# Kernel tuning notes

Measured on AMD Instinct MI355X. Metric: run time of the kernel, lower is better.

The kernel has to match this reference:

```python
import jax, jax.numpy as jnp
import numpy as np

DIM = 384
WS = 8        # window_size
SHIFT = 4     # shift_size
HEADS = 8
HEAD_DIM = DIM // HEADS
SCALE = HEAD_DIM ** (-0.5)
EPS = 1e-5


def layernorm(x, g, b):
    m = jnp.mean(x, axis=-1, keepdims=True)
    v = jnp.var(x, axis=-1, keepdims=True)
    return (x - m) * jax.lax.rsqrt(v + EPS) * g + b


def setup_inputs() -> dict:
    key = jax.random.key(0)
    ks = jax.random.split(key, 8)
    s = 0.02
    return {
        "x": jax.random.normal(ks[0], (8, DIM, 64, 64), dtype=jnp.float32),
        "qkv_w": jax.random.normal(ks[1], (DIM, 3 * DIM), dtype=jnp.float32) * s,
        "qkv_b": jnp.zeros((3 * DIM,), jnp.float32),
        "proj_w": jax.random.normal(ks[2], (DIM, DIM), dtype=jnp.float32) * s,
        "proj_b": jnp.zeros((DIM,), jnp.float32),
        "ln1_g": jnp.ones((DIM,), jnp.float32),
        "ln1_b": jnp.zeros((DIM,), jnp.float32),
        "ln2_g": jnp.ones((DIM,), jnp.float32),
        "ln2_b": jnp.zeros((DIM,), jnp.float32),
        "mlp_w1": jax.random.normal(ks[3], (DIM, 4 * DIM), dtype=jnp.float32) * s,
        "mlp_b1": jnp.zeros((4 * DIM,), jnp.float32),
        "mlp_w2": jax.random.normal(ks[4], (4 * DIM, DIM), dtype=jnp.float32) * s,
        "mlp_b2": jnp.zeros((DIM,), jnp.float32),
    }


def reference(x, qkv_w, qkv_b, proj_w, proj_b, ln1_g, ln1_b, ln2_g, ln2_b,
              mlp_w1, mlp_b1, mlp_w2, mlp_b2):
    B, C, H, W = x.shape
    x_skip = jnp.transpose(x, (0, 2, 3, 1))  # [B,H,W,C]
    xh = x_skip
    pad_b = (-H) % WS
    pad_r = (-W) % WS
    xh = jnp.pad(xh, ((0, 0), (0, pad_b), (0, pad_r), (0, 0)))
    Hp, Wp = xh.shape[1], xh.shape[2]
    if SHIFT > 0:
        xh = jnp.roll(xh, (-SHIFT, -SHIFT), axis=(1, 2))
    # window partition -> [B*nH*nW, WS*WS, C]
    win = xh.reshape(B, Hp // WS, WS, Wp // WS, WS, C)
    win = win.transpose(0, 1, 3, 2, 4, 5).reshape(-1, WS * WS, C)
    win = layernorm(win, ln1_g, ln1_b)
    # windowed MHA (no shift mask in original module)
    Bw, N, _ = win.shape
    qkv = (win @ qkv_w + qkv_b).reshape(Bw, N, 3, HEADS, HEAD_DIM)
    qkv = qkv.transpose(2, 0, 3, 1, 4)  # [3, Bw, H, N, d]
    q, k, v = qkv[0] * SCALE, qkv[1], qkv[2]
    attn = jax.nn.softmax(jnp.einsum('bhnd,bhmd->bhnm', q, k), axis=-1)
    out = jnp.einsum('bhnm,bhmd->bhnd', attn, v)
    out = out.transpose(0, 2, 1, 3).reshape(Bw, N, C)
    out = out @ proj_w + proj_b
    # window reverse
    xh = out.reshape(B, Hp // WS, Wp // WS, WS, WS, C)
    xh = xh.transpose(0, 1, 3, 2, 4, 5).reshape(B, Hp, Wp, C)
    if SHIFT > 0:
        xh = jnp.roll(xh, (SHIFT, SHIFT), axis=(1, 2))
    xh = xh[:, :H, :W, :] + x_skip
    h = layernorm(xh, ln2_g, ln2_b)
    h = jax.nn.gelu(h @ mlp_w1 + mlp_b1, approximate=False) @ mlp_w2 + mlp_b2
    return jnp.transpose(h, (0, 3, 1, 2))  # [B,C,H,W]
```

## Files before the change

### kernel.cpp

```cpp
#include <hip/hip_runtime.h>
#include <hip/hip_bf16.h>
#include <math.h>

#define DIM   384
#define HEADS 8
#define HD    48
#define NTOK  32768
#define NWIN  512

typedef __attribute__((ext_vector_type(8))) short bf16x8;
typedef __attribute__((ext_vector_type(8))) unsigned short u16x8;
typedef __attribute__((ext_vector_type(4))) float f32x4;

__device__ __forceinline__ float bf2f(unsigned short u) {
    unsigned int v = ((unsigned int)u) << 16;
    return __uint_as_float(v);
}
__device__ __forceinline__ unsigned short f2bf(float f) {
    __bf16 b = (__bf16)f;
    return __builtin_bit_cast(unsigned short, b);
}

__device__ __forceinline__ float gelu(float v) {
    float z  = v * 0.70710678118654752f;
    float az = fabsf(z);
    float t  = __builtin_amdgcn_rcpf(1.0f + 0.47047f * az);
    float p  = t * (0.3480242f + t * (-0.0958798f + t * 0.7478556f));
    float ea = 1.0f - p * __expf(-az * az);
    float er = copysignf(ea, z);
    return 0.5f * v * (1.0f + er);
}

__device__ __forceinline__ void tok2src(int tok, int& b, int& hs, int& ws) {
    int bb  = tok >> 12;
    int win = (tok >> 6) & 63;
    int t   = tok & 63;
    int hi = win >> 3, wi = win & 7;
    int r  = t >> 3,  cc = t & 7;
    b  = bb;
    hs = (hi * 8 + r  + 4) & 63;
    ws = (wi * 8 + cc + 4) & 63;
}

__global__ __launch_bounds__(256) void k_wt4(const float* __restrict__ qkv_w,
                                             const float* __restrict__ proj_w,
                                             const float* __restrict__ w1,
                                             const float* __restrict__ w2,
                                             unsigned short* __restrict__ d0,
                                             unsigned short* __restrict__ d1,
                                             unsigned short* __restrict__ d2,
                                             unsigned short* __restrict__ d3) {
    __shared__ unsigned short T[64][66];
    int b = blockIdx.x;
    const float* W; unsigned short* Wt; int K, N, lt;
    if (b < 108)      { W = qkv_w;  Wt = d0; K = 384;  N = 1152; lt = b; }
    else if (b < 144) { W = proj_w; Wt = d1; K = 384;  N = 384;  lt = b - 108; }
    else if (b < 288) { W = w1;     Wt = d2; K = 384;  N = 1536; lt = b - 144; }
    else              { W = w2;     Wt = d3; K = 1536; N = 384;  lt = b - 288; }
    int tn = N >> 6;
    int k0 = (lt / tn) << 6, n0 = (lt % tn) << 6;
    int t  = threadIdx.x;
    int cl = t & 63, rw = t >> 6;
    #pragma unroll
    for (int p = 0; p < 16; p++) {
        int kk = p * 4 + rw;
        T[cl][kk] = f2bf(W[(size_t)(k0 + kk) * N + n0 + cl]);
    }
    __syncthreads();
    #pragma unroll
    for (int p = 0; p < 16; p++) {
        int nn = p * 4 + rw;
        Wt[(size_t)(n0 + nn) * K + k0 + cl] = T[nn][cl];
    }
}

__global__ __launch_bounds__(256) void k_ln1(const float* __restrict__ x,
                                             const float* __restrict__ g,
                                             const float* __restrict__ bt,
                                             unsigned short* __restrict__ ln1) {
    int blk = blockIdx.x;
    int b  = blk >> 6, hs = blk & 63;
    int t  = threadIdx.x;
    int w  = t & 63, cg = t >> 6;
    const float* row = x + (size_t)b * DIM * 4096 + hs * 64;

    float v[96];
    float sum = 0.f, sq = 0.f;
    #pragma unroll
    for (int i = 0; i < 96; i++) {
        int c = i * 4 + cg;
        float xv = row[(size_t)c * 4096 + w];
        v[i] = xv;
        sum += xv; sq += xv * xv;
    }
    __shared__ float red[2][4][64];
    __shared__ float mean_s[64], rstd_s[64];
    red[0][cg][w] = sum; red[1][cg][w] = sq;
    __syncthreads();
    if (t < 64) {
        float s  = red[0][0][t] + red[0][1][t] + red[0][2][t] + red[0][3][t];
        float q2 = red[1][0][t] + red[1][1][t] + red[1][2][t] + red[1][3][t];
        float mean = s * (1.0f / DIM);
        float var  = q2 * (1.0f / DIM) - mean * mean;
        mean_s[t] = mean;
        rstd_s[t] = rsqrtf(var + 1e-5f);
    }
    __syncthreads();

    int wp = t >> 2, seg = t & 3;
    int hr = (hs + 60) & 63, wr = (wp + 60) & 63;
    int tok = ((b * 8 + (hr >> 3)) * 8 + (wr >> 3)) * 64 + (hr & 7) * 8 + (wr & 7);

    __shared__ __align__(16) unsigned short tile[64][72];
    #pragma unroll
    for (int chunk = 0; chunk < 6; chunk++) {
        float mean = mean_s[w], rstd = rstd_s[w];
        #pragma unroll
        for (int it = 0; it < 16; it++) {
            int cl = it * 4 + cg;
            int c  = chunk * 64 + cl;
            tile[w][cl] = f2bf((v[chunk * 16 + it] - mean) * rstd * g[c] + bt[c]);
        }
        __syncthreads();
        u16x8 v0 = *(const u16x8*)&tile[wp][seg * 16];
        u16x8 v1 = *(const u16x8*)&tile[wp][seg * 16 + 8];
        unsigned short* op = ln1 + (size_t)tok * DIM + chunk * 64 + seg * 16;
        *(u16x8*)op = v0;
        *(u16x8*)(op + 8) = v1;
        __syncthreads();
    }
}

template <int EPI, int K>
__global__ __launch_bounds__(256) void k_gemm_mfma(
        const unsigned short* __restrict__ A,
        const unsigned short* __restrict__ Bt,
        const float* __restrict__ bias,
        void* __restrict__ Cout,
        const float* __restrict__ xres,
        int N, int GX) {
    __shared__ __align__(16) unsigned short SH[24576];
    int tid  = threadIdx.x;
    int lane = tid & 63;
    int wave = tid >> 6;
    int wm = wave >> 1, wn = wave & 1;
    int quad = lane >> 4, l15 = lane & 15;

    int l   = blockIdx.x;
    int xcd = l & 7;
    int r_  = l >> 3;
    int bx  = r_ % GX;
    int by  = (r_ / GX) * 8 + xcd;
    int m0 = by * 128, n0 = bx * 128;

    const unsigned short* gA0 = A  + (size_t)(m0 +      lane) * K + wave * 8;
    const unsigned short* gA1 = A  + (size_t)(m0 + 64 + lane) * K + wave * 8;
    const unsigned short* gB0 = Bt + (size_t)(n0 +      lane) * K + wave * 8;
    const unsigned short* gB1 = Bt + (size_t)(n0 + 64 + lane) * K + wave * 8;

    auto stage = [&](int buf) {
        __builtin_amdgcn_global_load_lds(
            (const __attribute__((address_space(1))) void*)gA0,
            (__attribute__((address_space(3))) void*)&SH[buf * 4096 + wave * 1024],
            16, 0, 0);
        __builtin_amdgcn_global_load_lds(
            (const __attribute__((address_space(1))) void*)gA1,
            (__attribute__((address_space(3))) void*)&SH[buf * 4096 + wave * 1024 + 512],
            16, 0, 0);
        __builtin_amdgcn_global_load_lds(
            (const __attribute__((address_space(1))) void*)gB0,
            (__attribute__((address_space(3))) void*)&SH[12288 + buf * 4096 + wave * 1024],
            16, 0, 0);
        __builtin_amdgcn_global_load_lds(
            (const __attribute__((address_space(1))) void*)gB1,
            (__attribute__((address_space(3))) void*)&SH[12288 + buf * 4096 + wave * 1024 + 512],
            16, 0, 0);
        gA0 += 32; gA1 += 32; gB0 += 32; gB1 += 32;
    };

    f32x4 acc[4][4] = {};
    constexpr int NSTEPS = K >> 5;
    constexpr int U = NSTEPS / 3;

    int oa = (quad * 128 + wm * 64 + l15) * 8;
    int ob = 12288 + (quad * 128 + wn * 64 + l15) * 8;

    stage(0);
    stage(1);

#define GSTEP(CUR, NXT, MODE)                                                \
    {                                                                        \
        __builtin_amdgcn_s_barrier();                                        \
        if constexpr ((MODE) == 0) {                                         \
            stage(NXT);                                                      \
            asm volatile("s_waitcnt vmcnt(8)" ::: "memory");                 \
        } else if constexpr ((MODE) == 1) {                                  \
            asm volatile("s_waitcnt vmcnt(4)" ::: "memory");                 \
        } else {                                                             \
            asm volatile("s_waitcnt vmcnt(0)" ::: "memory");                 \
        }                                                                    \
        __builtin_amdgcn_s_barrier();                                        \
        bf16x8 af[4], bfr[4];                                                \
        _Pragma("unroll")                                                    \
        for (int r = 0; r < 4; r++)                                          \
            af[r] = *(const bf16x8*)&SH[(CUR) * 4096 + oa + r * 128];        \
        _Pragma("unroll")                                                    \
        for (int r2 = 0; r2 < 4; r2++)                                       \
            bfr[r2] = *(const bf16x8*)&SH[(CUR) * 4096 + ob + r2 * 128];     \
        _Pragma("unroll")                                                    \
        for (int r = 0; r < 4; r++)                                          \
            _Pragma("unroll")                                                \
            for (int r2 = 0; r2 < 4; r2++)                                   \
                acc[r][r2] = __builtin_amdgcn_mfma_f32_16x16x32_bf16(        \
                                 af[r], bfr[r2], acc[r][r2], 0, 0, 0);       \
    }

    #pragma unroll 1
    for (int u = 0; u < U - 1; ++u) {
        GSTEP(0, 2, 0)
        GSTEP(1, 0, 0)
        GSTEP(2, 1, 0)
    }
    GSTEP(0, 2, 0)
    GSTEP(1, 0, 1)
    GSTEP(2, 0, 2)
#undef GSTEP

    if constexpr (EPI == 2 || EPI == 3) {
        #pragma unroll
        for (int r2 = 0; r2 < 4; r2++) {
            int n = n0 + wn * 64 + r2 * 16 + l15;
            float bn = bias[n];
            #pragma unroll
            for (int r = 0; r < 4; r++) {
                #pragma unroll
                for (int reg = 0; reg < 4; reg++) {
                    int m = m0 + wm * 64 + r * 16 + quad * 4 + reg;
                    float v = acc[r][r2][reg] + bn;
                    if (EPI == 2) {
                        int b, hs, ws_;
                        tok2src(m, b, hs, ws_);
                        v += xres[(((size_t)b * DIM + n) * 64 + hs) * 64 + ws_];
                        int p = (b * 64 + hs) * 64 + ws_;
                        ((float*)Cout)[(size_t)p * N + n] = v;
                    } else {
                        ((float*)Cout)[(size_t)m * N + n] = v;
                    }
                }
            }
        }
    } else if constexpr (EPI == 5) {
        float* SF = (float*)SH;
        __syncthreads();
        int b   = m0 >> 12;
        int hs0 = (m0 >> 6) & 63;
        #pragma unroll
        for (int h2 = 0; h2 < 2; h2++) {
            if (wm == h2) {
                #pragma unroll
                for (int r2 = 0; r2 < 4; r2++) {
                    int c = wn * 64 + r2 * 16 + l15;
                    float bn = bias[n0 + c];
                    #pragma unroll
                    for (int r = 0; r < 4; r++) {
                        f32x4 v4;
                        #pragma unroll
                        for (int reg = 0; reg < 4; reg++)
                            v4[reg] = acc[r][r2][reg] + bn;
                        *(f32x4*)&SF[c * 68 + r * 16 + quad * 4] = v4;
                    }
                }
            }
            __syncthreads();
            #pragma unroll
            for (int i = 0; i < 8; i++) {
                int id = tid + i * 256;
                int c  = id >> 4, ch = id & 15;
                f32x4 v = *(const f32x4*)&SF[c * 68 + ch * 4];
                float* dst = (float*)Cout + ((size_t)(b * DIM + n0 + c) * 64 + hs0 + h2) * 64;
                *(f32x4*)&dst[ch * 4] = v;
            }
            __syncthreads();
        }
    } else {
        __syncthreads();
        #pragma unroll
        for (int r2 = 0; r2 < 4; r2++) {
            int col = wn * 64 + r2 * 16 + l15;
            float bn = bias[n0 + col];
            #pragma unroll
            for (int r = 0; r < 4; r++) {
                int row0 = wm * 64 + r * 16 + quad * 4;
                #pragma unroll
                for (int reg = 0; reg < 4; reg++) {
                    int row = row0 + reg;
                    float v = acc[r][r2][reg] + bn;
                    if (EPI == 1) v = gelu(v);
                    SH[(row * 136 + col) ^ (((row >> 3) & 1) << 4)] = f2bf(v);
                }
            }
        }
        __syncthreads();
        #pragma unroll
        for (int i = 0; i < 8; i++) {
            int chunk = tid + i * 256;
            int m = chunk >> 4, nc = chunk & 15;
            int idx = (m * 136 + nc * 8) ^ (((m >> 3) & 1) << 4);
            u16x8 v = *(const u16x8*)&SH[idx];
            if (EPI == 4) {
                int n = n0 + nc * 8;
                int qi  = n / 384;
                int rem = n - qi * 384;
                int hh  = rem / 48;
                int d   = rem - hh * 48;
                *(u16x8*)&((unsigned short*)Cout)[((size_t)(qi * 8 + hh) * NTOK + m0 + m) * 48 + d] = v;
            } else {
                *(u16x8*)&((unsigned short*)Cout)[(size_t)(m0 + m) * N + n0 + nc * 8] = v;
            }
        }
    }
}

__global__ __launch_bounds__(256) void k_attn_mfma(
        const unsigned short* __restrict__ qkvh,
        unsigned short* __restrict__ attn) {
    __shared__ __align__(16) unsigned short lds[4][8064];
    int tid  = threadIdx.x;
    int lane = tid & 63;
    int wave = tid >> 6;
    int quad = lane >> 4, l15 = lane & 15;
    int win  = blockIdx.x;
    int tok0 = win * 64;
    unsigned short* VT = &lds[wave][0];
    unsigned short* P  = &lds[wave][3456];
    const float scale = 0.14433756729740643f;

    for (int hi = 0; hi < 2; hi++) {
        int h = wave + hi * 4;
        const unsigned short* qb = qkvh + ((size_t)(0 * 8 + h) * NTOK + tok0) * 48;
        const unsigned short* kb = qkvh + ((size_t)(1 * 8 + h) * NTOK + tok0) * 48;
        const unsigned short* vb = qkvh + ((size_t)(2 * 8 + h) * NTOK + tok0) * 48;

        #pragma unroll
        for (int i = 0; i < 6; i++) {
            u16x8 v = *(const u16x8*)&vb[lane * 48 + i * 8];
            #pragma unroll
            for (int j = 0; j < 8; j++)
                VT[(i * 8 + j) * 72 + lane] = v[j];
        }

        bf16x8 kf[4][2];
        #pragma unroll
        for (int ni = 0; ni < 4; ni++) {
            kf[ni][0] = *(const bf16x8*)&kb[(ni * 16 + l15) * 48 + quad * 8];
            bf16x8 z = {};
            if (quad < 2)
                z = *(const bf16x8*)&kb[(ni * 16 + l15) * 48 + 32 + quad * 8];
            kf[ni][1] = z;
        }

        f32x4 sacc[4][4] = {};
        #pragma unroll
        for (int mi = 0; mi < 4; mi++) {
            bf16x8 qf0 = *(const bf16x8*)&qb[(mi * 16 + l15) * 48 + quad * 8];
            bf16x8 qf1 = {};
            if (quad < 2)
                qf1 = *(const bf16x8*)&qb[(mi * 16 + l15) * 48 + 32 + quad * 8];
            #pragma unroll
            for (int ni = 0; ni < 4; ni++) {
                sacc[mi][ni] = __builtin_amdgcn_mfma_f32_16x16x32_bf16(qf0, kf[ni][0], sacc[mi][ni], 0, 0, 0);
                sacc[mi][ni] = __builtin_amdgcn_mfma_f32_16x16x32_bf16(qf1, kf[ni][1], sacc[mi][ni], 0, 0, 0);
            }
        }

        #pragma unroll
        for (int mi = 0; mi < 4; mi++) {
            #pragma unroll
            for (int reg = 0; reg < 4; reg++) {
                float s0 = sacc[mi][0][reg] * scale;
                float s1 = sacc[mi][1][reg] * scale;
                float s2 = sacc[mi][2][reg] * scale;
                float s3 = sacc[mi][3][reg] * scale;
                float mx = fmaxf(fmaxf(s0, s1), fmaxf(s2, s3));
                #pragma unroll
                for (int off = 1; off < 16; off <<= 1)
                    mx = fmaxf(mx, __shfl_xor(mx, off));
                float e0 = __expf(s0 - mx);
                float e1 = __expf(s1 - mx);
                float e2 = __expf(s2 - mx);
                float e3 = __expf(s3 - mx);
                float sm = e0 + e1 + e2 + e3;
                #pragma unroll
                for (int off = 1; off < 16; off <<= 1)
                    sm += __shfl_xor(sm, off);
                float inv = 1.0f / sm;
                int row = mi * 16 + quad * 4 + reg;
                P[row * 72 +  0 + l15] = f2bf(e0 * inv);
                P[row * 72 + 16 + l15] = f2bf(e1 * inv);
                P[row * 72 + 32 + l15] = f2bf(e2 * inv);
                P[row * 72 + 48 + l15] = f2bf(e3 * inv);
            }
        }

        bf16x8 vf[3][2];
        #pragma unroll
        for (int ni = 0; ni < 3; ni++)
            #pragma unroll
            for (int kt = 0; kt < 2; kt++)
                vf[ni][kt] = *(const bf16x8*)&VT[(ni * 16 + l15) * 72 + kt * 32 + quad * 8];

        #pragma unroll
        for (int mi = 0; mi < 4; mi++) {
            bf16x8 pf0 = *(const bf16x8*)&P[(mi * 16 + l15) * 72 + quad * 8];
            bf16x8 pf1 = *(const bf16x8*)&P[(mi * 16 + l15) * 72 + 32 + quad * 8];
            f32x4 o[3] = {};
            #pragma unroll
            for (int ni = 0; ni < 3; ni++) {
                o[ni] = __builtin_amdgcn_mfma_f32_16x16x32_bf16(pf0, vf[ni][0], o[ni], 0, 0, 0);
                o[ni] = __builtin_amdgcn_mfma_f32_16x16x32_bf16(pf1, vf[ni][1], o[ni], 0, 0, 0);
            }
            #pragma unroll
            for (int ni = 0; ni < 3; ni++)
                #pragma unroll
                for (int reg = 0; reg < 4; reg++) {
                    int tok = tok0 + mi * 16 + quad * 4 + reg;
                    attn[(size_t)tok * DIM + h * HD + ni * 16 + l15] = f2bf(o[ni][reg]);
                }
        }
    }
}

__global__ __launch_bounds__(64) void k_ln2(const float* __restrict__ y,
                                            const float* __restrict__ g,
                                            const float* __restrict__ bt,
                                            unsigned short* __restrict__ out) {
    int tok = blockIdx.x;
    int t   = threadIdx.x;
    const float* row = y + (size_t)tok * DIM;
    float v[6];
    float sum = 0.f, sq = 0.f;
    #pragma unroll
    for (int i = 0; i < 6; i++) {
        v[i] = row[i * 64 + t];
        sum += v[i]; sq += v[i] * v[i];
    }
    #pragma unroll
    for (int o = 32; o > 0; o >>= 1) {
        sum += __shfl_xor(sum, o, 64);
        sq  += __shfl_xor(sq, o, 64);
    }
    float mean = sum * (1.0f / DIM);
    float var  = sq * (1.0f / DIM) - mean * mean;
    float rstd = rsqrtf(var + 1e-5f);
    unsigned short* orow = out + (size_t)tok * DIM;
    #pragma unroll
    for (int i = 0; i < 6; i++) {
        int c = i * 64 + t;
        orow[c] = f2bf((v[i] - mean) * rstd * g[c] + bt[c]);
    }
}

extern "C" void kernel_launch(void* const* d_in, const int* in_sizes, int n_in,
                              void* d_out, int out_size, void* d_ws, size_t ws_size,
                              hipStream_t stream) {
    const float* x      = (const float*)d_in[0];
    const float* qkv_w  = (const float*)d_in[1];
    const float* qkv_b  = (const float*)d_in[2];
    const float* proj_w = (const float*)d_in[3];
    const float* proj_b = (const float*)d_in[4];
    const float* ln1_g  = (const float*)d_in[5];
    const float* ln1_b  = (const float*)d_in[6];
    const float* ln2_g  = (const float*)d_in[7];
    const float* ln2_b  = (const float*)d_in[8];
    const float* w1     = (const float*)d_in[9];
    const float* b1     = (const float*)d_in[10];
    const float* w2     = (const float*)d_in[11];
    const float* b2     = (const float*)d_in[12];

    char* ws = (char*)d_ws;
    unsigned short* qkv_wt  = (unsigned short*)(ws + 0);
    unsigned short* proj_wt = (unsigned short*)(ws + 884736);
    unsigned short* w1t     = (unsigned short*)(ws + 1179648);
    unsigned short* w2t     = (unsigned short*)(ws + 2359296);
    unsigned short* ln1     = (unsigned short*)(ws + 4194304);
    unsigned short* qkv     = (unsigned short*)(ws + 29360128);
    unsigned short* attn    = (unsigned short*)(ws + 104857600);
    float*          y       = (float*)(ws + 130023424);
    unsigned short* ln2     = ln1;
    unsigned short* mid     = qkv;

    k_wt4<<<432, 256, 0, stream>>>(qkv_w, proj_w, w1, w2, qkv_wt, proj_wt, w1t, w2t);
    k_ln1<<<512, 256, 0, stream>>>(x, ln1_g, ln1_b, ln1);
    k_gemm_mfma<4, 384><<<9 * 256, 256, 0, stream>>>(ln1, qkv_wt, qkv_b, qkv, nullptr, 1152, 9);
    k_attn_mfma<<<NWIN, 256, 0, stream>>>(qkv, attn);
    k_gemm_mfma<2, 384><<<3 * 256, 256, 0, stream>>>(attn, proj_wt, proj_b, y, x, 384, 3);
    k_ln2<<<NTOK, 64, 0, stream>>>(y, ln2_g, ln2_b, ln2);
    k_gemm_mfma<1, 384><<<12 * 256, 256, 0, stream>>>(ln2, w1t, b1, mid, nullptr, 1536, 12);
    k_gemm_mfma<5, 1536><<<3 * 256, 256, 0, stream>>>(mid, w2t, b2, (float*)d_out, nullptr, 384, 3);
}
```

Before: 425.2 us.

## Fuse window attention, output projection, residual add and LayerNorm2 into one kernel

The attention kernel now keeps each window's 64x384 attention output in shared memory and runs the output projection GEMM directly from it, with proj weights read from global memory and prefetched one k-step ahead. It then adds the bias and residual, computes LayerNorm2 statistics with a cross-wave shared-memory reduction, and writes the bf16 LN2 output in token order. This removes the attn and fp32 y intermediate round trips through global memory and two kernel launches. In exchange there is more shared memory per block, launch bounds of one block per SM, only 512 blocks, and uncoalesced strided reads of x for the residual.

```diff
diff --git a/kernel.cpp b/kernel.cpp
--- a/kernel.cpp
+++ b/kernel.cpp
@@ -226,7 +226,7 @@
     GSTEP(2, 0, 2)
 #undef GSTEP
 
-    if constexpr (EPI == 2 || EPI == 3) {
+    if constexpr (EPI == 3) {
         #pragma unroll
         for (int r2 = 0; r2 < 4; r2++) {
             int n = n0 + wn * 64 + r2 * 16 + l15;
@@ -236,16 +236,7 @@
                 #pragma unroll
                 for (int reg = 0; reg < 4; reg++) {
                     int m = m0 + wm * 64 + r * 16 + quad * 4 + reg;
-                    float v = acc[r][r2][reg] + bn;
-                    if (EPI == 2) {
-                        int b, hs, ws_;
-                        tok2src(m, b, hs, ws_);
-                        v += xres[(((size_t)b * DIM + n) * 64 + hs) * 64 + ws_];
-                        int p = (b * 64 + hs) * 64 + ws_;
-                        ((float*)Cout)[(size_t)p * N + n] = v;
-                    } else {
-                        ((float*)Cout)[(size_t)m * N + n] = v;
-                    }
+                    ((float*)Cout)[(size_t)m * N + n] = acc[r][r2][reg] + bn;
                 }
             }
         }
@@ -321,10 +312,18 @@
     }
 }
 
-__global__ __launch_bounds__(256) void k_attn_mfma(
+__global__ __launch_bounds__(256, 1) void k_fused(
         const unsigned short* __restrict__ qkvh,
-        unsigned short* __restrict__ attn) {
+        const unsigned short* __restrict__ proj_wt,
+        const float* __restrict__ proj_b,
+        const float* __restrict__ x,
+        const float* __restrict__ ln2_g,
+        const float* __restrict__ ln2_b,
+        unsigned short* __restrict__ out) {
     __shared__ __align__(16) unsigned short lds[4][8064];
+    __shared__ __align__(16) unsigned short AT[64][392];
+    __shared__ float red[2][4][64];
+    __shared__ float mrs[2][64];
     int tid  = threadIdx.x;
     int lane = tid & 63;
     int wave = tid >> 6;
@@ -422,41 +421,112 @@
             #pragma unroll
             for (int ni = 0; ni < 3; ni++)
                 #pragma unroll
-                for (int reg = 0; reg < 4; reg++) {
-                    int tok = tok0 + mi * 16 + quad * 4 + reg;
-                    attn[(size_t)tok * DIM + h * HD + ni * 16 + l15] = f2bf(o[ni][reg]);
-                }
-        }
-    }
-}
-
-__global__ __launch_bounds__(64) void k_ln2(const float* __restrict__ y,
-                                            const float* __restrict__ g,
-                                            const float* __restrict__ bt,
-                                            unsigned short* __restrict__ out) {
-    int tok = blockIdx.x;
-    int t   = threadIdx.x;
-    const float* row = y + (size_t)tok * DIM;
-    float v[6];
-    float sum = 0.f, sq = 0.f;
-    #pragma unroll
-    for (int i = 0; i < 6; i++) {
-        v[i] = row[i * 64 + t];
-        sum += v[i]; sq += v[i] * v[i];
-    }
-    #pragma unroll
-    for (int o = 32; o > 0; o >>= 1) {
-        sum += __shfl_xor(sum, o, 64);
-        sq  += __shfl_xor(sq, o, 64);
-    }
-    float mean = sum * (1.0f / DIM);
-    float var  = sq * (1.0f / DIM) - mean * mean;
-    float rstd = rsqrtf(var + 1e-5f);
-    unsigned short* orow = out + (size_t)tok * DIM;
-    #pragma unroll
-    for (int i = 0; i < 6; i++) {
-        int c = i * 64 + t;
-        orow[c] = f2bf((v[i] - mean) * rstd * g[c] + bt[c]);
+                for (int reg = 0; reg < 4; reg++)
+                    AT[mi * 16 + quad * 4 + reg][h * HD + ni * 16 + l15] = f2bf(o[ni][reg]);
+        }
+    }
+    __syncthreads();
+
+    f32x4 pacc[4][6] = {};
+    const unsigned short* Bw = proj_wt + (size_t)(wave * 96) * 384;
+    bf16x8 bcur[6], bnxt[6];
+    #pragma unroll
+    for (int nj = 0; nj < 6; nj++)
+        bcur[nj] = *(const bf16x8*)&Bw[(nj * 16 + l15) * 384 + quad * 8];
+    #pragma unroll 1
+    for (int ks = 0; ks < 12; ++ks) {
+        if (ks + 1 < 12) {
+            #pragma unroll
+            for (int nj = 0; nj < 6; nj++)
+                bnxt[nj] = *(const bf16x8*)&Bw[(nj * 16 + l15) * 384 + (ks + 1) * 32 + quad * 8];
+        }
+        bf16x8 a[4];
+        #pragma unroll
+        for (int mi = 0; mi < 4; mi++)
+            a[mi] = *(const bf16x8*)&AT[mi * 16 + l15][ks * 32 + quad * 8];
+        #pragma unroll
+        for (int mi = 0; mi < 4; mi++)
+            #pragma unroll
+            for (int nj = 0; nj < 6; nj++)
+                pacc[mi][nj] = __builtin_amdgcn_mfma_f32_16x16x32_bf16(
+                                   a[mi], bcur[nj], pacc[mi][nj], 0, 0, 0);
+        #pragma unroll
+        for (int nj = 0; nj < 6; nj++) bcur[nj] = bnxt[nj];
+    }
+
+    #pragma unroll
+    for (int mi = 0; mi < 4; mi++) {
+        #pragma unroll
+        for (int reg = 0; reg < 4; reg++) {
+            int tok = tok0 + mi * 16 + quad * 4 + reg;
+            int b, hs, ws_;
+            tok2src(tok, b, hs, ws_);
+            const float* xr = x + (((size_t)b * DIM) * 64 + hs) * 64 + ws_;
+            #pragma unroll
+            for (int nj = 0; nj < 6; nj++) {
+                int c = wave * 96 + nj * 16 + l15;
+                pacc[mi][nj][reg] += proj_b[c] + xr[(size_t)c * 4096];
+            }
+        }
+    }
+
+    #pragma unroll
+    for (int mi = 0; mi < 4; mi++) {
+        #pragma unroll
+        for (int reg = 0; reg < 4; reg++) {
+            float s = 0.f, q = 0.f;
+            #pragma unroll
+            for (int nj = 0; nj < 6; nj++) {
+                float v = pacc[mi][nj][reg];
+                s += v; q += v * v;
+            }
+            #pragma unroll
+            for (int off = 1; off < 16; off <<= 1) {
+                s += __shfl_xor(s, off);
+                q += __shfl_xor(q, off);
+            }
+            if (l15 == 0) {
+                int row = mi * 16 + quad * 4 + reg;
+                red[0][wave][row] = s;
+                red[1][wave][row] = q;
+            }
+        }
+    }
+    __syncthreads();
+    if (tid < 64) {
+        float s = red[0][0][tid] + red[0][1][tid] + red[0][2][tid] + red[0][3][tid];
+        float q = red[1][0][tid] + red[1][1][tid] + red[1][2][tid] + red[1][3][tid];
+        float mean = s * (1.0f / DIM);
+        float var  = q * (1.0f / DIM) - mean * mean;
+        mrs[0][tid] = mean;
+        mrs[1][tid] = rsqrtf(var + 1e-5f);
+    }
+    __syncthreads();
+
+    #pragma unroll
+    for (int mi = 0; mi < 4; mi++) {
+        #pragma unroll
+        for (int nj = 0; nj < 6; nj++) {
+            int c = wave * 96 + nj * 16 + l15;
+            float gg = ln2_g[c], bb = ln2_b[c];
+            #pragma unroll
+            for (int reg = 0; reg < 4; reg++) {
+                int row = mi * 16 + quad * 4 + reg;
+                float v = (pacc[mi][nj][reg] - mrs[0][row]) * mrs[1][row] * gg + bb;
+                AT[row][c] = f2bf(v);
+            }
+        }
+    }
+    __syncthreads();
+    #pragma unroll
+    for (int i = 0; i < 12; i++) {
+        int id  = tid + i * 256;
+        int row = id / 48, ch = id - row * 48;
+        int b, hs, ws_;
+        tok2src(tok0 + row, b, hs, ws_);
+        int p = (b * 64 + hs) * 64 + ws_;
+        u16x8 v = *(const u16x8*)&AT[row][ch * 8];
+        *(u16x8*)&out[(size_t)p * DIM + ch * 8] = v;
     }
 }
 
@@ -484,17 +554,13 @@
     unsigned short* w2t     = (unsigned short*)(ws + 2359296);
     unsigned short* ln1     = (unsigned short*)(ws + 4194304);
     unsigned short* qkv     = (unsigned short*)(ws + 29360128);
-    unsigned short* attn    = (unsigned short*)(ws + 104857600);
-    float*          y       = (float*)(ws + 130023424);
     unsigned short* ln2     = ln1;
     unsigned short* mid     = qkv;
 
     k_wt4<<<432, 256, 0, stream>>>(qkv_w, proj_w, w1, w2, qkv_wt, proj_wt, w1t, w2t);
     k_ln1<<<512, 256, 0, stream>>>(x, ln1_g, ln1_b, ln1);
     k_gemm_mfma<4, 384><<<9 * 256, 256, 0, stream>>>(ln1, qkv_wt, qkv_b, qkv, nullptr, 1152, 9);
-    k_attn_mfma<<<NWIN, 256, 0, stream>>>(qkv, attn);
-    k_gemm_mfma<2, 384><<<3 * 256, 256, 0, stream>>>(attn, proj_wt, proj_b, y, x, 384, 3);
-    k_ln2<<<NTOK, 64, 0, stream>>>(y, ln2_g, ln2_b, ln2);
+    k_fused<<<NWIN, 256, 0, stream>>>(qkv, proj_wt, proj_b, x, ln2_g, ln2_b, ln2);
     k_gemm_mfma<1, 384><<<12 * 256, 256, 0, stream>>>(ln2, w1t, b1, mid, nullptr, 1536, 12);
     k_gemm_mfma<5, 1536><<<3 * 256, 256, 0, stream>>>(mid, w2t, b2, (float*)d_out, nullptr, 384, 3);
 }
```

Result: slower. 441.2 us (+3.8%).
